# Kernel optimization log

Measured on AMD Instinct MI355X. Metric: run time of the kernel, lower is better.

Reference implementation:

```python
import jax, jax.numpy as jnp
import numpy as np

N_NODES = 50000
N_EDGES = 800000
D_IN = 64
D_OUT = 64


def setup_inputs() -> dict:
    key = jax.random.key(0)
    k1, k2, k3, k4, k5 = jax.random.split(key, 5)
    features = jax.random.normal(k1, (N_NODES, D_IN), dtype=jnp.float32)
    edge_src = jax.random.randint(k2, (N_EDGES,), 0, N_NODES, dtype=jnp.int32)
    edge_dst = jax.random.randint(k3, (N_EDGES,), 0, N_NODES, dtype=jnp.int32)
    edge_weight = jax.random.uniform(k4, (N_EDGES,), dtype=jnp.float32)
    # Linear(2*D_IN, D_OUT): weight [D_OUT, 2*D_IN], bias [D_OUT]
    W = jax.random.normal(k5, (D_OUT, 2 * D_IN), dtype=jnp.float32) * (1.0 / np.sqrt(2 * D_IN))
    b = jnp.zeros((D_OUT,), dtype=jnp.float32)
    return {"features": features, "edge_src": edge_src, "edge_dst": edge_dst,
            "edge_weight": edge_weight, "W": W, "b": b}


def reference(features, edge_src, edge_dst, edge_weight, W, b):
    n = features.shape[0]
    # spmm(adj, features): out[i] = sum_j adj[i,j] * features[j]
    gathered = features[edge_src] * edge_weight[:, None]          # [E, D_IN]
    neighbor = jax.ops.segment_sum(gathered, edge_dst, num_segments=n)  # [N, D_IN]
    combined = jnp.concatenate([features, neighbor], axis=1)     # [N, 2*D_IN]
    out = combined @ W.T + b                                      # [N, D_OUT]
    # F.normalize(p=2, dim=1): x / max(||x||, 1e-12)
    norm = jnp.maximum(jnp.linalg.norm(out, axis=1, keepdims=True), 1e-12)
    return out / norm
```

## Files before the change

### kernel.cpp

```cpp
#include <hip/hip_runtime.h>

#define D 64
#define TILE 1024
#define RB 8
#define EPT 4
#define CHUNK_E (256 * EPT)

__device__ __forceinline__ float rlane(float v, int l) {
    return __int_as_float(__builtin_amdgcn_readlane(__float_as_int(v), l));
}

__global__ __launch_bounds__(256) void hist_kernel(
    const int* __restrict__ edge_dst, int* __restrict__ deg,
    int n_edges, int n_nodes)
{
    int r = blockIdx.x & (RB - 1);
    int chunk = blockIdx.x >> 3;
    int lo = (int)((long long)r * n_nodes / RB);
    int hi = (int)((long long)(r + 1) * n_nodes / RB);
    int base = chunk * CHUNK_E + threadIdx.x * EPT;
    int d[EPT];
    if (base + EPT - 1 < n_edges) {
        int4 v = *(const int4*)(edge_dst + base);
        d[0] = v.x; d[1] = v.y; d[2] = v.z; d[3] = v.w;
    } else {
        #pragma unroll
        for (int k = 0; k < EPT; ++k)
            d[k] = (base + k < n_edges) ? edge_dst[base + k] : -1;
    }
    #pragma unroll
    for (int k = 0; k < EPT; ++k)
        if (d[k] >= lo && d[k] < hi) atomicAdd(&deg[d[k]], 1);
}

__global__ __launch_bounds__(256) void tile_sum_kernel(
    const int* __restrict__ deg, int* __restrict__ partial, int n)
{
    int t = threadIdx.x;
    int base = blockIdx.x * TILE + t * 4;
    int s = 0;
    if (base + 3 < n) {
        int4 v = *(const int4*)(deg + base);
        s = v.x + v.y + v.z + v.w;
    } else {
        for (int k = 0; k < 4; ++k) if (base + k < n) s += deg[base + k];
    }
    #pragma unroll
    for (int off = 1; off < 64; off <<= 1) s += __shfl_xor(s, off, 64);
    __shared__ int wsum[4];
    int lane = t & 63, wv = t >> 6;
    if (lane == 0) wsum[wv] = s;
    __syncthreads();
    if (t == 0) partial[blockIdx.x] = wsum[0] + wsum[1] + wsum[2] + wsum[3];
}

__global__ __launch_bounds__(64) void scan_partial_kernel(
    const int* __restrict__ partial, int* __restrict__ ppref, int nb,
    int* __restrict__ offsets, int n, int n_edges)
{
    int lane = threadIdx.x;
    int carry = 0;
    for (int base = 0; base < nb; base += 64) {
        int idx = base + lane;
        int v = (idx < nb) ? partial[idx] : 0;
        int inc = v;
        #pragma unroll
        for (int off = 1; off < 64; off <<= 1) {
            int u = __shfl_up(inc, off, 64);
            if (lane >= off) inc += u;
        }
        if (idx < nb) ppref[idx] = carry + inc - v;
        carry += __shfl(inc, 63, 64);
    }
    if (lane == 0) offsets[n] = n_edges;
}

__global__ __launch_bounds__(256) void scan_tile_kernel(
    const int* __restrict__ deg, const int* __restrict__ ppref,
    int* __restrict__ offsets, int* __restrict__ cursor, int n)
{
    int t = threadIdx.x;
    int base = blockIdx.x * TILE + t * 4;
    int e0 = 0, e1 = 0, e2 = 0, e3 = 0;
    if (base + 3 < n) {
        int4 v = *(const int4*)(deg + base);
        e0 = v.x; e1 = v.y; e2 = v.z; e3 = v.w;
    } else {
        if (base + 0 < n) e0 = deg[base + 0];
        if (base + 1 < n) e1 = deg[base + 1];
        if (base + 2 < n) e2 = deg[base + 2];
        if (base + 3 < n) e3 = deg[base + 3];
    }
    int s = e0 + e1 + e2 + e3;
    int inc = s;
    int lane = t & 63, wv = t >> 6;
    #pragma unroll
    for (int off = 1; off < 64; off <<= 1) {
        int u = __shfl_up(inc, off, 64);
        if (lane >= off) inc += u;
    }
    __shared__ int wsum[4];
    if (lane == 63) wsum[wv] = inc;
    __syncthreads();
    int wpre = 0;
    for (int wq = 0; wq < wv; ++wq) wpre += wsum[wq];
    int excl = ppref[blockIdx.x] + wpre + inc - s;
    int o0 = excl, o1 = o0 + e0, o2 = o1 + e1, o3 = o2 + e2;
    if (base + 0 < n) { offsets[base + 0] = o0; cursor[base + 0] = o0; }
    if (base + 1 < n) { offsets[base + 1] = o1; cursor[base + 1] = o1; }
    if (base + 2 < n) { offsets[base + 2] = o2; cursor[base + 2] = o2; }
    if (base + 3 < n) { offsets[base + 3] = o3; cursor[base + 3] = o3; }
}

__global__ __launch_bounds__(256) void fill_kernel(
    const int* __restrict__ edge_src, const int* __restrict__ edge_dst,
    const float* __restrict__ edge_weight,
    int* __restrict__ cursor, int2* __restrict__ csr_sw,
    int n_edges, int n_nodes)
{
    int r = blockIdx.x & (RB - 1);
    int chunk = blockIdx.x >> 3;
    int lo = (int)((long long)r * n_nodes / RB);
    int hi = (int)((long long)(r + 1) * n_nodes / RB);
    int base = chunk * CHUNK_E + threadIdx.x * EPT;
    int d[EPT];
    if (base + EPT - 1 < n_edges) {
        int4 v = *(const int4*)(edge_dst + base);
        d[0] = v.x; d[1] = v.y; d[2] = v.z; d[3] = v.w;
    } else {
        #pragma unroll
        for (int k = 0; k < EPT; ++k)
            d[k] = (base + k < n_edges) ? edge_dst[base + k] : -1;
    }
    #pragma unroll
    for (int k = 0; k < EPT; ++k) {
        int dk = d[k];
        if (dk >= lo && dk < hi) {
            int e = base + k;
            int pos = atomicAdd(&cursor[dk], 1);
            csr_sw[pos] = make_int2(edge_src[e], __float_as_int(edge_weight[e]));
        }
    }
}

__global__ __launch_bounds__(256) void gather_kernel(
    const float* __restrict__ features, const int2* __restrict__ csr_sw,
    const int* __restrict__ offsets, float* __restrict__ neighbor, int n_nodes)
{
    int lane = threadIdx.x & 63;
    int gw = (blockIdx.x * 256 + threadIdx.x) >> 6;
    int nw = (gridDim.x * 256) >> 6;
    for (int i = gw; i < n_nodes; i += nw) {
        int beg = __builtin_amdgcn_readfirstlane(offsets[i]);
        int end = __builtin_amdgcn_readfirstlane(offsets[i + 1]);
        float acc = 0.f;
        int j = beg;
        for (; j + 7 < end; j += 8) {
            int2 p[8];
            float a[8];
            #pragma unroll
            for (int q = 0; q < 8; ++q) p[q] = csr_sw[j + q];
            #pragma unroll
            for (int q = 0; q < 8; ++q)
                a[q] = features[(size_t)p[q].x * D + lane];
            #pragma unroll
            for (int q = 0; q < 8; ++q)
                acc = fmaf(__int_as_float(p[q].y), a[q], acc);
        }
        for (; j < end; ++j) {
            int2 p = csr_sw[j];
            acc = fmaf(__int_as_float(p.y), features[(size_t)p.x * D + lane], acc);
        }
        neighbor[(size_t)i * D + lane] = acc;
    }
}

__global__ __launch_bounds__(256) void gemm_norm_kernel(
    const float* __restrict__ features, const float* __restrict__ neighbor,
    const float* __restrict__ W, const float* __restrict__ bias,
    float* __restrict__ out, int n_nodes)
{
    int lane = threadIdx.x & 63;
    float wr[128];
    const float4* Wv = (const float4*)(W + (size_t)lane * 128);
    #pragma unroll
    for (int q = 0; q < 32; ++q) {
        float4 v = Wv[q];
        wr[4 * q + 0] = v.x; wr[4 * q + 1] = v.y;
        wr[4 * q + 2] = v.z; wr[4 * q + 3] = v.w;
    }
    float bl = bias[lane];

    int gw = (blockIdx.x * 256 + threadIdx.x) >> 6;
    int nw = (gridDim.x * 256) >> 6;
    for (int i = gw; i < n_nodes; i += nw) {
        float cf = features[(size_t)i * D + lane];
        float cn = neighbor[(size_t)i * D + lane];
        float acc = bl;
        #pragma unroll
        for (int k = 0; k < 64; ++k)
            acc = fmaf(rlane(cf, k), wr[k], acc);
        #pragma unroll
        for (int k = 0; k < 64; ++k)
            acc = fmaf(rlane(cn, k), wr[64 + k], acc);
        float s = acc * acc;
        #pragma unroll
        for (int m = 1; m < 64; m <<= 1) s += __shfl_xor(s, m, 64);
        out[(size_t)i * D + lane] = acc / fmaxf(sqrtf(s), 1e-12f);
    }
}

extern "C" void kernel_launch(void* const* d_in, const int* in_sizes, int n_in,
                              void* d_out, int out_size, void* d_ws, size_t ws_size,
                              hipStream_t stream) {
    const float* features    = (const float*)d_in[0];
    const int*   edge_src    = (const int*)d_in[1];
    const int*   edge_dst    = (const int*)d_in[2];
    const float* edge_weight = (const float*)d_in[3];
    const float* W           = (const float*)d_in[4];
    const float* b           = (const float*)d_in[5];
    float*       out         = (float*)d_out;

    int n = in_sizes[0] / D;
    int E = in_sizes[1];
    int nb = (n + TILE - 1) / TILE;
    int nchunks = (E + CHUNK_E - 1) / CHUNK_E;

    char* ws = (char*)d_ws;
    auto al = [](size_t x) { return (x + 255) & ~(size_t)255; };
    size_t o = 0;
    int* deg      = (int*)(ws + o); o += al((size_t)n * 4);
    int* cursor   = (int*)(ws + o); o += al((size_t)n * 4);
    int* offsets  = (int*)(ws + o); o += al((size_t)(n + 1) * 4);
    int* partial  = (int*)(ws + o); o += al((size_t)nb * 4);
    int* ppref    = (int*)(ws + o); o += al((size_t)nb * 4);
    int2* csr_sw  = (int2*)(ws + o); o += al((size_t)E * 8);
    float* neighbor = (float*)(ws + o);

    hipMemsetAsync(deg, 0, (size_t)n * 4, stream);

    hist_kernel<<<nchunks * RB, 256, 0, stream>>>(edge_dst, deg, E, n);
    tile_sum_kernel<<<nb, 256, 0, stream>>>(deg, partial, n);
    scan_partial_kernel<<<1, 64, 0, stream>>>(partial, ppref, nb, offsets, n, E);
    scan_tile_kernel<<<nb, 256, 0, stream>>>(deg, ppref, offsets, cursor, n);
    fill_kernel<<<nchunks * RB, 256, 0, stream>>>(edge_src, edge_dst, edge_weight,
                                                  cursor, csr_sw, E, n);
    gather_kernel<<<2048, 256, 0, stream>>>(features, csr_sw, offsets,
                                            neighbor, n);
    gemm_norm_kernel<<<1024, 256, 0, stream>>>(features, neighbor, W, b, out, n);
}
```

Baseline: 227.8 us.

## Compact in-range edges via wave ballot into LDS before global atomics

The histogram and fill kernels now load 8 edges per thread (2048 per block). They use wave ballots and an LDS counter to compact the edges whose destination falls in the block's range into shared memory, then issue the global atomics from the compacted list. This keeps lanes busy instead of mostly masked out, since only 1/8 of edges fall in each range. The GEMM-norm kernel splits its FMA chain into four independent accumulators to cut dependency latency, and its grid doubles to 2048 blocks. The trade-off is an extra LDS pass and syncthreads, plus a changed floating-point summation order.

```diff
diff --git a/kernel.cpp b/kernel.cpp
--- a/kernel.cpp
+++ b/kernel.cpp
@@ -3,8 +3,8 @@
 #define D 64
 #define TILE 1024
 #define RB 8
-#define EPT 4
-#define CHUNK_E (256 * EPT)
+#define EPB 2048
+#define EPT 8
 
 __device__ __forceinline__ float rlane(float v, int l) {
     return __int_as_float(__builtin_amdgcn_readlane(__float_as_int(v), l));
@@ -14,23 +14,46 @@
     const int* __restrict__ edge_dst, int* __restrict__ deg,
     int n_edges, int n_nodes)
 {
+    __shared__ int s_cnt;
+    __shared__ int s_d[EPB];
     int r = blockIdx.x & (RB - 1);
     int chunk = blockIdx.x >> 3;
     int lo = (int)((long long)r * n_nodes / RB);
     int hi = (int)((long long)(r + 1) * n_nodes / RB);
-    int base = chunk * CHUNK_E + threadIdx.x * EPT;
+    if (threadIdx.x == 0) s_cnt = 0;
+    __syncthreads();
+
+    int base = chunk * EPB + threadIdx.x * EPT;
     int d[EPT];
     if (base + EPT - 1 < n_edges) {
-        int4 v = *(const int4*)(edge_dst + base);
-        d[0] = v.x; d[1] = v.y; d[2] = v.z; d[3] = v.w;
+        int4 v0 = *(const int4*)(edge_dst + base);
+        int4 v1 = *(const int4*)(edge_dst + base + 4);
+        d[0]=v0.x; d[1]=v0.y; d[2]=v0.z; d[3]=v0.w;
+        d[4]=v1.x; d[5]=v1.y; d[6]=v1.z; d[7]=v1.w;
     } else {
         #pragma unroll
         for (int k = 0; k < EPT; ++k)
             d[k] = (base + k < n_edges) ? edge_dst[base + k] : -1;
     }
-    #pragma unroll
-    for (int k = 0; k < EPT; ++k)
-        if (d[k] >= lo && d[k] < hi) atomicAdd(&deg[d[k]], 1);
+
+    int lane = threadIdx.x & 63;
+    unsigned long long lt = (lane == 63) ? ~0ull >> 1
+                                         : ((1ull << (lane + 1)) - 1) >> 1;
+    #pragma unroll
+    for (int k = 0; k < EPT; ++k) {
+        bool m = (d[k] >= lo && d[k] < hi);
+        unsigned long long bal = __ballot(m);
+        int cw = __popcll(bal);
+        if (cw) {
+            int bs = 0;
+            if (lane == 0) bs = atomicAdd(&s_cnt, cw);
+            bs = __builtin_amdgcn_readfirstlane(bs);
+            if (m) s_d[bs + __popcll(bal & lt)] = d[k];
+        }
+    }
+    __syncthreads();
+    int c = s_cnt;
+    for (int i = threadIdx.x; i < c; i += 256) atomicAdd(&deg[s_d[i]], 1);
 }
 
 __global__ __launch_bounds__(256) void tile_sum_kernel(
@@ -118,28 +141,55 @@
     int* __restrict__ cursor, int2* __restrict__ csr_sw,
     int n_edges, int n_nodes)
 {
+    __shared__ int s_cnt;
+    __shared__ int s_d[EPB];
+    __shared__ int s_e[EPB];
     int r = blockIdx.x & (RB - 1);
     int chunk = blockIdx.x >> 3;
     int lo = (int)((long long)r * n_nodes / RB);
     int hi = (int)((long long)(r + 1) * n_nodes / RB);
-    int base = chunk * CHUNK_E + threadIdx.x * EPT;
+    if (threadIdx.x == 0) s_cnt = 0;
+    __syncthreads();
+
+    int base = chunk * EPB + threadIdx.x * EPT;
     int d[EPT];
     if (base + EPT - 1 < n_edges) {
-        int4 v = *(const int4*)(edge_dst + base);
-        d[0] = v.x; d[1] = v.y; d[2] = v.z; d[3] = v.w;
+        int4 v0 = *(const int4*)(edge_dst + base);
+        int4 v1 = *(const int4*)(edge_dst + base + 4);
+        d[0]=v0.x; d[1]=v0.y; d[2]=v0.z; d[3]=v0.w;
+        d[4]=v1.x; d[5]=v1.y; d[6]=v1.z; d[7]=v1.w;
     } else {
         #pragma unroll
         for (int k = 0; k < EPT; ++k)
             d[k] = (base + k < n_edges) ? edge_dst[base + k] : -1;
     }
+
+    int lane = threadIdx.x & 63;
+    unsigned long long lt = (lane == 63) ? ~0ull >> 1
+                                         : ((1ull << (lane + 1)) - 1) >> 1;
     #pragma unroll
     for (int k = 0; k < EPT; ++k) {
-        int dk = d[k];
-        if (dk >= lo && dk < hi) {
-            int e = base + k;
-            int pos = atomicAdd(&cursor[dk], 1);
-            csr_sw[pos] = make_int2(edge_src[e], __float_as_int(edge_weight[e]));
-        }
+        bool m = (d[k] >= lo && d[k] < hi);
+        unsigned long long bal = __ballot(m);
+        int cw = __popcll(bal);
+        if (cw) {
+            int bs = 0;
+            if (lane == 0) bs = atomicAdd(&s_cnt, cw);
+            bs = __builtin_amdgcn_readfirstlane(bs);
+            if (m) {
+                int p = bs + __popcll(bal & lt);
+                s_d[p] = d[k];
+                s_e[p] = base + k;
+            }
+        }
+    }
+    __syncthreads();
+    int c = s_cnt;
+    for (int i = threadIdx.x; i < c; i += 256) {
+        int dk = s_d[i];
+        int e  = s_e[i];
+        int pos = atomicAdd(&cursor[dk], 1);
+        csr_sw[pos] = make_int2(edge_src[e], __float_as_int(edge_weight[e]));
     }
 }
 
@@ -196,13 +246,15 @@
     for (int i = gw; i < n_nodes; i += nw) {
         float cf = features[(size_t)i * D + lane];
         float cn = neighbor[(size_t)i * D + lane];
-        float acc = bl;
-        #pragma unroll
-        for (int k = 0; k < 64; ++k)
-            acc = fmaf(rlane(cf, k), wr[k], acc);
-        #pragma unroll
-        for (int k = 0; k < 64; ++k)
-            acc = fmaf(rlane(cn, k), wr[64 + k], acc);
+        float a0 = bl, a1 = 0.f, a2 = 0.f, a3 = 0.f;
+        #pragma unroll
+        for (int k = 0; k < 32; ++k) {
+            a0 = fmaf(rlane(cf, k),      wr[k],      a0);
+            a1 = fmaf(rlane(cf, k + 32), wr[k + 32], a1);
+            a2 = fmaf(rlane(cn, k),      wr[k + 64], a2);
+            a3 = fmaf(rlane(cn, k + 32), wr[k + 96], a3);
+        }
+        float acc = (a0 + a1) + (a2 + a3);
         float s = acc * acc;
         #pragma unroll
         for (int m = 1; m < 64; m <<= 1) s += __shfl_xor(s, m, 64);
@@ -224,7 +276,7 @@
     int n = in_sizes[0] / D;
     int E = in_sizes[1];
     int nb = (n + TILE - 1) / TILE;
-    int nchunks = (E + CHUNK_E - 1) / CHUNK_E;
+    int nchunks = (E + EPB - 1) / EPB;
 
     char* ws = (char*)d_ws;
     auto al = [](size_t x) { return (x + 255) & ~(size_t)255; };
@@ -247,5 +299,5 @@
                                                   cursor, csr_sw, E, n);
     gather_kernel<<<2048, 256, 0, stream>>>(features, csr_sw, offsets,
                                             neighbor, n);
-    gemm_norm_kernel<<<1024, 256, 0, stream>>>(features, neighbor, W, b, out, n);
-}
+    gemm_norm_kernel<<<2048, 256, 0, stream>>>(features, neighbor, W, b, out, n);
+}
```

Result: no change. 230.4 us (+1.1%).
